# Performance work log

Hardware: AMD Instinct MI355X
Metric: run time of the kernel (lower is better)

Reference implementation:

```python
import jax, jax.numpy as jnp
import numpy as np

B, S, D, H = 1, 2048, 4096, 32
HD = D // H  # 128


def _rope_params(seq_len, head_dim, base=10000.0):
    inv_freq = 1.0 / (base ** (np.arange(0, head_dim, 2, dtype=np.float64) / head_dim))
    ang = np.outer(np.arange(seq_len, dtype=np.float64), inv_freq)      # [S, HD/2]
    ang = np.concatenate([ang, ang], axis=-1)                            # [S, HD]
    return jnp.asarray(np.cos(ang), jnp.float32), jnp.asarray(np.sin(ang), jnp.float32)


def _apply_rope(x, cos, sin):
    # x: [B, H, S, HD]; cos/sin: [S, HD]
    half = x.shape[-1] // 2
    x1, x2 = x[..., :half], x[..., half:]
    rotated = jnp.concatenate([-x2, x1], axis=-1)
    return x * cos[None, None] + rotated * sin[None, None]


def setup_inputs() -> dict:
    key = jax.random.key(0)
    ks = jax.random.split(key, 6)
    w_scale = 1.0 / np.sqrt(D)
    X = jax.random.normal(ks[0], (B, S, D), jnp.float32)
    Wq = jax.random.normal(ks[1], (D, D), jnp.float32) * w_scale
    Wk = jax.random.normal(ks[2], (D, D), jnp.float32) * w_scale
    Wv = jax.random.normal(ks[3], (D, D), jnp.float32) * w_scale
    Wo = jax.random.normal(ks[4], (D, D), jnp.float32) * w_scale
    bo = jax.random.normal(ks[5], (D,), jnp.float32) * 0.01
    cos, sin = _rope_params(S, HD)
    return {"X": X, "Wq": Wq, "Wk": Wk, "Wv": Wv, "Wo": Wo, "bo": bo, "cos": cos, "sin": sin}


def reference(X, Wq, Wk, Wv, Wo, bo, cos, sin):
    b, s, d = X.shape
    # nn.Linear: y = x @ W.T
    def split_heads(y):
        return y.reshape(b, s, H, HD).transpose(0, 2, 1, 3)  # [B,H,S,HD]
    q = split_heads(X @ Wq.T)
    k = split_heads(X @ Wk.T)
    v = split_heads(X @ Wv.T)
    q = _apply_rope(q, cos, sin)
    k = _apply_rope(k, cos, sin)
    scores = jnp.einsum('bhqd,bhkd->bhqk', q, k) / np.sqrt(HD).astype(np.float32)
    causal = jnp.tril(jnp.ones((s, s), bool))
    scores = jnp.where(causal[None, None], scores, -jnp.inf)
    attn = jax.nn.softmax(scores, axis=-1)
    out = jnp.einsum('bhqk,bhkd->bhqd', attn, v)  # [B,H,S,HD]
    out = out.transpose(0, 2, 1, 3).reshape(b, s, d)
    return out @ Wo.T + bo
```

## Files before the change

kernel.cpp:

```cpp
#include <hip/hip_runtime.h>

typedef unsigned short u16;
typedef __attribute__((ext_vector_type(8))) short s16x8;
typedef __attribute__((ext_vector_type(4))) float f32x4;

__device__ __forceinline__ u16 f2bf(float f) {
  unsigned u = __float_as_uint(f);
  u += 0x7fffu + ((u >> 16) & 1u);
  return (u16)(u >> 16);
}
__device__ __forceinline__ float bf2f(u16 h) {
  return __uint_as_float(((unsigned)h) << 16);
}

typedef __attribute__((address_space(1))) const void gvoid_t;
typedef __attribute__((address_space(3))) void lvoid_t;
__device__ __forceinline__ void gload_lds16(const void* g, void* l) {
  __builtin_amdgcn_global_load_lds((gvoid_t*)g, (lvoid_t*)l, 16, 0, 0);
}

__global__ void cvt_f32_bf16(const float* __restrict__ in, u16* __restrict__ out, int n) {
  int i = (blockIdx.x * 256 + threadIdx.x) * 4;
  if (i >= n) return;
  float4 v = *(const float4*)(in + i);
  ushort4 o;
  o.x = f2bf(v.x); o.y = f2bf(v.y); o.z = f2bf(v.z); o.w = f2bf(v.w);
  *(ushort4*)(out + i) = o;
}

template<typename OutT, bool BIAS>
__global__ __launch_bounds__(512, 2) void gemm_bt2(
    const u16* __restrict__ A, const u16* __restrict__ Bm,
    OutT* __restrict__ C, const float* __restrict__ bias,
    int M, int N, int K)
{
  __shared__ u16 As[3][128 * 64];
  __shared__ u16 Bs[3][256 * 64];

  const int t = threadIdx.x;
  const int lane = t & 63, wid = t >> 6;
  const int wm = wid >> 2, wn = wid & 3;
  const int lr = lane & 15, lk = lane >> 4;

  const int wg = blockIdx.x;
  const int xcd = wg & 7, j = wg >> 3;
  const int m0 = (j & 15) * 128;
  const int n0 = ((xcd << 1) | (j >> 4)) * 256;

  const int nt = K >> 6;

  f32x4 acc[4][4] = {};

#define STAGE(KT)                                                              \
  {                                                                            \
    const int bu_ = ((unsigned)(KT)) % 3u;                                     \
    const int k0_ = (KT) << 6;                                                 \
    _Pragma("unroll")                                                          \
    for (int it = 0; it < 2; ++it) {                                           \
      int id = it * 512 + t;                                                   \
      int r = id >> 3, c0 = id & 7;                                            \
      gload_lds16(A + (size_t)(m0 + r) * K + k0_ + ((c0 ^ (r & 7)) << 3),      \
                  &As[bu_][id * 8]);                                           \
    }                                                                          \
    _Pragma("unroll")                                                          \
    for (int it = 0; it < 4; ++it) {                                           \
      int id = it * 512 + t;                                                   \
      int r = id >> 3, c0 = id & 7;                                            \
      gload_lds16(Bm + (size_t)(n0 + r) * K + k0_ + ((c0 ^ (r & 7)) << 3),     \
                  &Bs[bu_][id * 8]);                                           \
    }                                                                          \
  }

  STAGE(0);
  STAGE(1);
  asm volatile("s_waitcnt vmcnt(6)" ::: "memory");
  __builtin_amdgcn_s_barrier();

  for (int kt = 0; kt < nt; ++kt) {
    const int bu = ((unsigned)kt) % 3u;
    if (kt + 2 < nt) STAGE(kt + 2);

#pragma unroll
    for (int ks = 0; ks < 2; ++ks) {
      s16x8 af[4], bf[4];
#pragma unroll
      for (int i = 0; i < 4; ++i) {
        int ra = wm * 64 + i * 16 + lr;
        af[i] = *(const s16x8*)&As[bu][ra * 64 + (((ks * 4 + lk) ^ (ra & 7)) << 3)];
        int rb = wn * 64 + i * 16 + lr;
        bf[i] = *(const s16x8*)&Bs[bu][rb * 64 + (((ks * 4 + lk) ^ (rb & 7)) << 3)];
      }
      asm volatile("s_waitcnt lgkmcnt(0)" ::: "memory");
      __builtin_amdgcn_sched_barrier(0);
      __builtin_amdgcn_s_setprio(1);
#pragma unroll
      for (int i = 0; i < 4; ++i)
#pragma unroll
        for (int jn = 0; jn < 4; ++jn)
          acc[i][jn] = __builtin_amdgcn_mfma_f32_16x16x32_bf16(af[i], bf[jn], acc[i][jn], 0, 0, 0);
      __builtin_amdgcn_s_setprio(0);
    }

    if (kt + 2 < nt)       { asm volatile("s_waitcnt vmcnt(6)" ::: "memory"); }
    else if (kt + 2 == nt) { asm volatile("s_waitcnt vmcnt(0)" ::: "memory"); }
    if (kt + 1 < nt) __builtin_amdgcn_s_barrier();
  }
#undef STAGE

#pragma unroll
  for (int i = 0; i < 4; ++i) {
    int row_b = m0 + wm * 64 + i * 16 + lk * 4;
#pragma unroll
    for (int jn = 0; jn < 4; ++jn) {
      int col = n0 + wn * 64 + jn * 16 + lr;
      float bv = BIAS ? bias[col] : 0.f;
#pragma unroll
      for (int r = 0; r < 4; ++r) {
        float v = acc[i][jn][r] + bv;
        size_t off = (size_t)(row_b + r) * N + col;
        if constexpr (sizeof(OutT) == 2) ((u16*)C)[off] = f2bf(v);
        else                             ((float*)C)[off] = v;
      }
    }
  }
}

__global__ void rope_qk(u16* __restrict__ Q, u16* __restrict__ Kt,
                        const float* __restrict__ cosp, const float* __restrict__ sinp) {
  int i = blockIdx.x * 256 + threadIdx.x;
  int d = i & 63;
  int h = (i >> 6) & 31;
  int s = i >> 11;
  float c = cosp[s * 128 + d], sn = sinp[s * 128 + d];
  size_t base = (size_t)s * 4096 + h * 128 + d;
  float q1 = bf2f(Q[base]), q2 = bf2f(Q[base + 64]);
  Q[base]      = f2bf(q1 * c - q2 * sn);
  Q[base + 64] = f2bf(q2 * c + q1 * sn);
  float k1 = bf2f(Kt[base]), k2 = bf2f(Kt[base + 64]);
  Kt[base]      = f2bf(k1 * c - k2 * sn);
  Kt[base + 64] = f2bf(k2 * c + k1 * sn);
}

__global__ __launch_bounds__(512) void flash_attn(
    const u16* __restrict__ Q, const u16* __restrict__ Kg, const u16* __restrict__ Vg,
    u16* __restrict__ Ctx)
{
  const int D = 4096;
  __shared__ u16 Ks[2][64 * 128];
  __shared__ u16 Vt[2][128 * 64];
  __shared__ u16 Ps[8][16 * 64];

  const int t = threadIdx.x, lane = t & 63, wid = t >> 6;
  const int lr = lane & 15, lk = lane >> 4;

  const int wg = blockIdx.x;
  const int xcd = wg & 7, j = wg >> 3;
  const int bx = 15 - (j >> 2);
  const int h = xcd * 4 + (j & 3);
  const int q0 = bx * 128;
  const int qw0 = q0 + wid * 16;

  s16x8 qf[4];
#pragma unroll
  for (int kc = 0; kc < 4; ++kc)
    qf[kc] = *(const s16x8*)(Q + (size_t)(qw0 + lr) * D + h * 128 + kc * 32 + lk * 8);

  f32x4 o[8] = {};
  float m_r[4] = {-1e30f, -1e30f, -1e30f, -1e30f};
  float l_r[4] = {0.f, 0.f, 0.f, 0.f};

  const int ntiles = 2 * bx + 2;
  const float scale2 = 0.12751779f;

  const int ch = t & 15, kv2 = (t >> 4) * 2;

  {
    const u16* src = Vg + (size_t)kv2 * D + h * 128 + ch * 8;
    s16x8 a0 = *(const s16x8*)src;
    s16x8 a1 = *(const s16x8*)(src + D);
#pragma unroll
    for (int it = 0; it < 2; ++it) {
      int id = it * 512 + t;
      int kv = id >> 4, c0 = id & 15;
      gload_lds16(Kg + (size_t)kv * D + h * 128 + ((c0 ^ (kv & 7)) << 3), &Ks[0][id * 8]);
    }
#pragma unroll
    for (int jj = 0; jj < 8; ++jj) {
      int d = ch * 8 + jj;
      int sw = ((ch ^ jj) & 7) << 3;
      unsigned pr = (unsigned)(u16)a0[jj] | ((unsigned)(u16)a1[jj] << 16);
      *(unsigned*)&Vt[0][d * 64 + (kv2 ^ sw)] = pr;
    }
  }

  for (int kt = 0; kt < ntiles; ++kt) {
    const int b = kt & 1;
    const int kv0 = kt * 64;
    __syncthreads();

    s16x8 a0, a1;
    const bool pf = (kt + 1 < ntiles);
    if (pf) {
      const u16* src = Vg + (size_t)(kv0 + 64 + kv2) * D + h * 128 + ch * 8;
      a0 = *(const s16x8*)src;
      a1 = *(const s16x8*)(src + D);
#pragma unroll
      for (int it = 0; it < 2; ++it) {
        int id = it * 512 + t;
        int kv = id >> 4, c0 = id & 15;
        gload_lds16(Kg + (size_t)(kv0 + 64 + kv) * D + h * 128 + ((c0 ^ (kv & 7)) << 3),
                    &Ks[b ^ 1][id * 8]);
      }
    }

    if (kv0 <= qw0 + 15) {
      const bool masked = (kv0 + 63 > qw0);

      f32x4 st[4] = {};
      __builtin_amdgcn_s_setprio(1);
#pragma unroll
      for (int nt = 0; nt < 4; ++nt) {
        int kv = nt * 16 + lr;
        int sw = kv & 7;
#pragma unroll
        for (int kc = 0; kc < 4; ++kc) {
          s16x8 kf = *(const s16x8*)&Ks[b][kv * 128 + (((4 * kc + lk) ^ sw) << 3)];
          st[nt] = __builtin_amdgcn_mfma_f32_16x16x32_bf16(qf[kc], kf, st[nt], 0, 0, 0);
        }
      }
      __builtin_amdgcn_s_setprio(0);

      float pmax_[4];
#pragma unroll
      for (int r = 0; r < 4; ++r) {
        int q_r = qw0 + lk * 4 + r;
        if (masked) {
#pragma unroll
          for (int nt = 0; nt < 4; ++nt) {
            float sv = st[nt][r] * scale2;
            if (kv0 + nt * 16 + lr > q_r) sv = -1e30f;
            st[nt][r] = sv;
          }
        } else {
#pragma unroll
          for (int nt = 0; nt < 4; ++nt) st[nt][r] *= scale2;
        }
        float pm = fmaxf(fmaxf(st[0][r], st[1][r]), fmaxf(st[2][r], st[3][r]));
        pm = fmaxf(pm, __shfl_xor(pm, 1));
        pm = fmaxf(pm, __shfl_xor(pm, 2));
        pm = fmaxf(pm, __shfl_xor(pm, 4));
        pm = fmaxf(pm, __shfl_xor(pm, 8));
        pmax_[r] = pm;
      }
      bool nr = (pmax_[0] > m_r[0] + 8.f) || (pmax_[1] > m_r[1] + 8.f) ||
                (pmax_[2] > m_r[2] + 8.f) || (pmax_[3] > m_r[3] + 8.f);
      if (__any(nr)) {
#pragma unroll
        for (int r = 0; r < 4; ++r) {
          float mn = fmaxf(m_r[r], pmax_[r]);
          float al = __builtin_amdgcn_exp2f(m_r[r] - mn);
          m_r[r] = mn; l_r[r] *= al;
#pragma unroll
          for (int nb = 0; nb < 8; ++nb) o[nb][r] *= al;
        }
      }
#pragma unroll
      for (int r = 0; r < 4; ++r) {
        int ql = lk * 4 + r;
        int swp = ((ql >> 1) & 7) << 3;
        float ps = 0.f;
#pragma unroll
        for (int nt = 0; nt < 4; ++nt) {
          float pv = __builtin_amdgcn_exp2f(st[nt][r] - m_r[r]);
          ps += pv;
          Ps[wid][ql * 64 + ((nt * 16 + lr) ^ swp)] = f2bf(pv);
        }
        ps += __shfl_xor(ps, 1);
        ps += __shfl_xor(ps, 2);
        ps += __shfl_xor(ps, 4);
        ps += __shfl_xor(ps, 8);
        l_r[r] += ps;
      }
      asm volatile("s_waitcnt lgkmcnt(0)" ::: "memory");

      s16x8 pa[2];
#pragma unroll
      for (int ks = 0; ks < 2; ++ks) {
        int col = (ks * 32 + lk * 8) ^ (((lr >> 1) & 7) << 3);
        pa[ks] = *(const s16x8*)&Ps[wid][lr * 64 + col];
      }

      __builtin_amdgcn_s_setprio(1);
#pragma unroll
      for (int ks = 0; ks < 2; ++ks) {
#pragma unroll
        for (int nb = 0; nb < 8; ++nb) {
          int d = nb * 16 + lr;
          int g = (((d >> 3) ^ d) & 7) << 3;
          s16x8 vf = *(const s16x8*)&Vt[b][d * 64 + ((ks * 32 + lk * 8) ^ g)];
          o[nb] = __builtin_amdgcn_mfma_f32_16x16x32_bf16(pa[ks], vf, o[nb], 0, 0, 0);
        }
      }
      __builtin_amdgcn_s_setprio(0);
    }

    if (pf) {
#pragma unroll
      for (int jj = 0; jj < 8; ++jj) {
        int d = ch * 8 + jj;
        int sw = ((ch ^ jj) & 7) << 3;
        unsigned pr = (unsigned)(u16)a0[jj] | ((unsigned)(u16)a1[jj] << 16);
        *(unsigned*)&Vt[b ^ 1][d * 64 + (kv2 ^ sw)] = pr;
      }
    }
  }

#pragma unroll
  for (int r = 0; r < 4; ++r) {
    float inv = 1.f / l_r[r];
    int q_r = qw0 + lk * 4 + r;
#pragma unroll
    for (int nb = 0; nb < 8; ++nb)
      Ctx[(size_t)q_r * D + h * 128 + nb * 16 + lr] = f2bf(o[nb][r] * inv);
  }
}

extern "C" void kernel_launch(void* const* d_in, const int* in_sizes, int n_in,
                              void* d_out, int out_size, void* d_ws, size_t ws_size,
                              hipStream_t stream) {
  const int S = 2048, D = 4096, H = 32;
  const size_t SD = (size_t)S * D, DD = (size_t)D * D;

  const float* X  = (const float*)d_in[0];
  const float* Wq = (const float*)d_in[1];
  const float* Wk = (const float*)d_in[2];
  const float* Wv = (const float*)d_in[3];
  const float* Wo = (const float*)d_in[4];
  const float* bo = (const float*)d_in[5];
  const float* cs = (const float*)d_in[6];
  const float* sn = (const float*)d_in[7];

  u16* WB = (u16*)d_ws;
  u16* Xb = WB + DD;
  u16* Qb = Xb + SD;
  u16* Kb = Qb + SD;
  u16* Vb = Kb + SD;

  dim3 blk(256);
  dim3 g2(256);
  dim3 b2(512);

  cvt_f32_bf16<<<(int)(SD / 1024), blk, 0, stream>>>(X, Xb, (int)SD);
  cvt_f32_bf16<<<(int)(DD / 1024), blk, 0, stream>>>(Wq, WB, (int)DD);
  gemm_bt2<u16, false><<<g2, b2, 0, stream>>>(Xb, WB, Qb, nullptr, S, D, D);
  cvt_f32_bf16<<<(int)(DD / 1024), blk, 0, stream>>>(Wk, WB, (int)DD);
  gemm_bt2<u16, false><<<g2, b2, 0, stream>>>(Xb, WB, Kb, nullptr, S, D, D);
  cvt_f32_bf16<<<(int)(DD / 1024), blk, 0, stream>>>(Wv, WB, (int)DD);
  gemm_bt2<u16, false><<<g2, b2, 0, stream>>>(Xb, WB, Vb, nullptr, S, D, D);

  rope_qk<<<(S * H * 64) / 256, blk, 0, stream>>>(Qb, Kb, cs, sn);

  flash_attn<<<dim3(512), dim3(512), 0, stream>>>(Qb, Kb, Vb, Xb );

  cvt_f32_bf16<<<(int)(DD / 1024), blk, 0, stream>>>(Wo, WB, (int)DD);
  gemm_bt2<float, true><<<g2, b2, 0, stream>>>(Xb, WB, (float*)d_out, bo, S, D, D);
}
```

Before: 581.0 us.

## Retile projection GEMMs to 128x128 tiles with 256 threads and K-step 32

```diff
diff --git a/kernel.cpp b/kernel.cpp
--- a/kernel.cpp
+++ b/kernel.cpp
@@ -29,83 +29,73 @@
 }
 
 template<typename OutT, bool BIAS>
-__global__ __launch_bounds__(512, 2) void gemm_bt2(
+__global__ __launch_bounds__(256) void gemm_bt3(
     const u16* __restrict__ A, const u16* __restrict__ Bm,
     OutT* __restrict__ C, const float* __restrict__ bias,
     int M, int N, int K)
 {
-  __shared__ u16 As[3][128 * 64];
-  __shared__ u16 Bs[3][256 * 64];
+  __shared__ u16 As[3][128 * 32];
+  __shared__ u16 Bs[3][128 * 32];
 
   const int t = threadIdx.x;
   const int lane = t & 63, wid = t >> 6;
-  const int wm = wid >> 2, wn = wid & 3;
+  const int wm = wid >> 1, wn = wid & 1;
   const int lr = lane & 15, lk = lane >> 4;
 
   const int wg = blockIdx.x;
   const int xcd = wg & 7, j = wg >> 3;
   const int m0 = (j & 15) * 128;
-  const int n0 = ((xcd << 1) | (j >> 4)) * 256;
-
-  const int nt = K >> 6;
+  const int n0 = ((xcd << 2) | (j >> 4)) * 128;
+
+  const int nt = K >> 5;
 
   f32x4 acc[4][4] = {};
 
-#define STAGE(KT)                                                              \
+#define STAGE3(KT)                                                             \
   {                                                                            \
-    const int bu_ = ((unsigned)(KT)) % 3u;                                     \
-    const int k0_ = (KT) << 6;                                                 \
+    const int bu_ = (KT) % 3;                                                  \
+    const int k0_ = (KT) << 5;                                                 \
     _Pragma("unroll")                                                          \
     for (int it = 0; it < 2; ++it) {                                           \
-      int id = it * 512 + t;                                                   \
-      int r = id >> 3, c0 = id & 7;                                            \
-      gload_lds16(A + (size_t)(m0 + r) * K + k0_ + ((c0 ^ (r & 7)) << 3),      \
-                  &As[bu_][id * 8]);                                           \
+      int id = it * 256 + t;                                                   \
+      int r = id >> 2, c0 = id & 3;                                            \
+      int cs = (c0 ^ ((r >> 1) & 3)) << 3;                                     \
+      gload_lds16(A + (size_t)(m0 + r) * K + k0_ + cs, &As[bu_][id * 8]);      \
+      gload_lds16(Bm + (size_t)(n0 + r) * K + k0_ + cs, &Bs[bu_][id * 8]);     \
     }                                                                          \
-    _Pragma("unroll")                                                          \
-    for (int it = 0; it < 4; ++it) {                                           \
-      int id = it * 512 + t;                                                   \
-      int r = id >> 3, c0 = id & 7;                                            \
-      gload_lds16(Bm + (size_t)(n0 + r) * K + k0_ + ((c0 ^ (r & 7)) << 3),     \
-                  &Bs[bu_][id * 8]);                                           \
-    }                                                                          \
-  }
-
-  STAGE(0);
-  STAGE(1);
-  asm volatile("s_waitcnt vmcnt(6)" ::: "memory");
+  }
+
+  STAGE3(0);
+  STAGE3(1);
+  asm volatile("s_waitcnt vmcnt(4)" ::: "memory");
   __builtin_amdgcn_s_barrier();
 
   for (int kt = 0; kt < nt; ++kt) {
-    const int bu = ((unsigned)kt) % 3u;
-    if (kt + 2 < nt) STAGE(kt + 2);
-
-#pragma unroll
-    for (int ks = 0; ks < 2; ++ks) {
-      s16x8 af[4], bf[4];
-#pragma unroll
-      for (int i = 0; i < 4; ++i) {
-        int ra = wm * 64 + i * 16 + lr;
-        af[i] = *(const s16x8*)&As[bu][ra * 64 + (((ks * 4 + lk) ^ (ra & 7)) << 3)];
-        int rb = wn * 64 + i * 16 + lr;
-        bf[i] = *(const s16x8*)&Bs[bu][rb * 64 + (((ks * 4 + lk) ^ (rb & 7)) << 3)];
-      }
-      asm volatile("s_waitcnt lgkmcnt(0)" ::: "memory");
-      __builtin_amdgcn_sched_barrier(0);
-      __builtin_amdgcn_s_setprio(1);
-#pragma unroll
-      for (int i = 0; i < 4; ++i)
-#pragma unroll
-        for (int jn = 0; jn < 4; ++jn)
-          acc[i][jn] = __builtin_amdgcn_mfma_f32_16x16x32_bf16(af[i], bf[jn], acc[i][jn], 0, 0, 0);
-      __builtin_amdgcn_s_setprio(0);
-    }
-
-    if (kt + 2 < nt)       { asm volatile("s_waitcnt vmcnt(6)" ::: "memory"); }
+    const int bu = kt % 3;
+    if (kt + 2 < nt) STAGE3(kt + 2);
+
+    s16x8 af[4], bf[4];
+#pragma unroll
+    for (int i = 0; i < 4; ++i) {
+      int ra = wm * 64 + i * 16 + lr;
+      af[i] = *(const s16x8*)&As[bu][ra * 32 + ((lk ^ ((ra >> 1) & 3)) << 3)];
+      int rb = wn * 64 + i * 16 + lr;
+      bf[i] = *(const s16x8*)&Bs[bu][rb * 32 + ((lk ^ ((rb >> 1) & 3)) << 3)];
+    }
+    __builtin_amdgcn_s_setprio(1);
+#pragma unroll
+    for (int i = 0; i < 4; ++i)
+#pragma unroll
+      for (int jn = 0; jn < 4; ++jn)
+        acc[i][jn] = __builtin_amdgcn_mfma_f32_16x16x32_bf16(af[i], bf[jn], acc[i][jn], 0, 0, 0);
+    __builtin_amdgcn_s_setprio(0);
+
+    asm volatile("s_waitcnt lgkmcnt(0)" ::: "memory");
+    if (kt + 2 < nt)       { asm volatile("s_waitcnt vmcnt(4)" ::: "memory"); }
     else if (kt + 2 == nt) { asm volatile("s_waitcnt vmcnt(0)" ::: "memory"); }
     if (kt + 1 < nt) __builtin_amdgcn_s_barrier();
   }
-#undef STAGE
+#undef STAGE3
 
 #pragma unroll
   for (int i = 0; i < 4; ++i) {
@@ -347,21 +337,21 @@
   u16* Vb = Kb + SD;
 
   dim3 blk(256);
-  dim3 g2(256);
-  dim3 b2(512);
+  dim3 g3(512);
+  dim3 b3(256);
 
   cvt_f32_bf16<<<(int)(SD / 1024), blk, 0, stream>>>(X, Xb, (int)SD);
   cvt_f32_bf16<<<(int)(DD / 1024), blk, 0, stream>>>(Wq, WB, (int)DD);
-  gemm_bt2<u16, false><<<g2, b2, 0, stream>>>(Xb, WB, Qb, nullptr, S, D, D);
+  gemm_bt3<u16, false><<<g3, b3, 0, stream>>>(Xb, WB, Qb, nullptr, S, D, D);
   cvt_f32_bf16<<<(int)(DD / 1024), blk, 0, stream>>>(Wk, WB, (int)DD);
-  gemm_bt2<u16, false><<<g2, b2, 0, stream>>>(Xb, WB, Kb, nullptr, S, D, D);
+  gemm_bt3<u16, false><<<g3, b3, 0, stream>>>(Xb, WB, Kb, nullptr, S, D, D);
   cvt_f32_bf16<<<(int)(DD / 1024), blk, 0, stream>>>(Wv, WB, (int)DD);
-  gemm_bt2<u16, false><<<g2, b2, 0, stream>>>(Xb, WB, Vb, nullptr, S, D, D);
+  gemm_bt3<u16, false><<<g3, b3, 0, stream>>>(Xb, WB, Vb, nullptr, S, D, D);
 
   rope_qk<<<(S * H * 64) / 256, blk, 0, stream>>>(Qb, Kb, cs, sn);
 
   flash_attn<<<dim3(512), dim3(512), 0, stream>>>(Qb, Kb, Vb, Xb );
 
   cvt_f32_bf16<<<(int)(DD / 1024), blk, 0, stream>>>(Wo, WB, (int)DD);
-  gemm_bt2<float, true><<<g2, b2, 0, stream>>>(Xb, WB, (float*)d_out, bo, S, D, D);
-}
+  gemm_bt3<float, true><<<g3, b3, 0, stream>>>(Xb, WB, (float*)d_out, bo, S, D, D);
+}
```

Measured after the change: 578.4 us. About the same (-0.4%).
